# Performance work log

Hardware: AMD Instinct MI355X
Metric: run time of the kernel (lower is better)

## Reference

```python
import jax, jax.numpy as jnp
import numpy as np

B, T, H = 64, 256, 128

def setup_inputs() -> dict:
    key = jax.random.key(0)
    ks = jax.random.split(key, 10)
    s = 1.0 / np.sqrt(H)
    return {
        "x": jax.random.normal(ks[0], (B, T, 2), jnp.float32),
        "enc_output": jax.random.normal(ks[1], (B, T, H), jnp.float32),
        "h0": jax.random.normal(ks[2], (B, H), jnp.float32) * s,
        "c0": jax.random.normal(ks[3], (B, H), jnp.float32) * s,
        "W1": jax.random.normal(ks[4], (H, H), jnp.float32) * s,
        "W2": jax.random.normal(ks[5], (H, H), jnp.float32) * s,
        "V": jax.random.normal(ks[6], (H,), jnp.float32) * s,
        "Wk": jax.random.normal(ks[7], (2, 4 * H), jnp.float32) * (1.0 / np.sqrt(2.0)),
        "Wr": jax.random.normal(ks[8], (H, 4 * H), jnp.float32) * s,
        "b": jnp.zeros((4 * H,), jnp.float32),
    }


def reference(x, enc_output, h0, c0, W1, W2, V, Wk, Wr, b):
    Bb, Tt, _ = x.shape
    # Precompute W1 @ enc_output once (original recomputes it T times inside K.rnn)
    enc_proj = jnp.einsum('bth,hk->btk', enc_output, W1)  # [B,T,H]

    def lstm_cell(inp, h, c):
        # Keras LSTMCell, gate order i,f,c,o; sigmoid recurrent activation, tanh activation
        z = inp @ Wk + h @ Wr + b  # [B,4H]
        zi, zf, zg, zo = jnp.split(z, 4, axis=-1)
        i = jax.nn.sigmoid(zi)
        f = jax.nn.sigmoid(zf)
        g = jnp.tanh(zg)
        o = jax.nn.sigmoid(zo)
        c_new = f * c + i * g
        h_new = o * jnp.tanh(c_new)
        return h_new, c_new

    def step(carry, _):
        h, c, ptr = carry
        h, c = lstm_cell(ptr, h, c)
        # additive attention over all encoder steps, batched (replaces inner K.rnn)
        scores = jnp.einsum('btk,k->bt', jnp.tanh(enc_proj + (h @ W2)[:, None, :]), V)
        probs = jax.nn.softmax(scores, axis=1)  # [B,T]
        # get_pointer with rank=0: top-1 of descending argsort == argmax
        idx = jnp.argmax(probs, axis=1)  # [B]
        ptr = jnp.take_along_axis(x, idx[:, None, None], axis=1)[:, 0, :]  # [B,2]
        return (h, c, ptr), probs

    ptr0 = jnp.ones((Bb, 2), x.dtype)
    _, probs_seq = jax.lax.scan(step, (h0, c0, ptr0), None, length=Tt)  # [T,B,T]
    return jnp.transpose(probs_seq, (1, 0, 2))  # [B,T,T]
```

## Files before the change

### kernel.cpp

```cpp
#include <hip/hip_runtime.h>
#include <cstddef>

#define TT 256
#define HH 128
#define EST 132
#define SCPS 260

__device__ __forceinline__ float rdlane(float v, int l) {
  return __int_as_float(__builtin_amdgcn_readlane(__float_as_int(v), l));
}
__device__ __forceinline__ float fast_sigmoid(float x) {
  const float L2E = 1.4426950408889634f;
  float y = __builtin_amdgcn_exp2f(-x * L2E);
  return __builtin_amdgcn_rcpf(1.0f + y);
}
__device__ __forceinline__ float fast_tanh(float x) {
  const float C2 = 2.8853900817779268f;
  float y = __builtin_amdgcn_exp2f(x * C2);
  return 1.0f - 2.0f * __builtin_amdgcn_rcpf(1.0f + y);
}

__global__ __attribute__((amdgpu_flat_work_group_size(512, 512),
                          amdgpu_waves_per_eu(2, 2)))
void decoder_kernel(const float* __restrict__ x,
                    const float* __restrict__ enc_output,
                    const float* __restrict__ h0,
                    const float* __restrict__ c0,
                    const float* __restrict__ W1,
                    const float* __restrict__ W2,
                    const float* __restrict__ V,
                    const float* __restrict__ Wk,
                    const float* __restrict__ Wr,
                    const float* __restrict__ bias,
                    float* __restrict__ out)
{
  __shared__ float E[TT * EST];
  __shared__ float zpart[4 * 512];
  __shared__ float scp[8 * SCPS];
  __shared__ float hbuf[HH];

  const int u    = threadIdx.x;
  const int b    = blockIdx.x;
  const int lane = u & 63;
  const int w    = u >> 6;
  const float C2  = 2.8853900817779268f;
  const float L2E = 1.4426950408889634f;

  {
    const float* encb = enc_output + (size_t)b * TT * HH;
    const int tsub = u >> 4;
    const int ks   = (u & 15) * 8;
    for (int p = 0; p < 8; ++p) {
      const int tt = p * 32 + tsub;
      float4 a0 = {0.f, 0.f, 0.f, 0.f};
      float4 a1 = {0.f, 0.f, 0.f, 0.f};
      const float4* er4 = (const float4*)(encb + tt * HH);
      for (int j4 = 0; j4 < 32; ++j4) {
        const float4 ev = er4[j4];
        const float* w1p = W1 + (j4 * 4) * HH + ks;
        float4 wa, wb;
        wa = *(const float4*)(w1p + 0 * HH); wb = *(const float4*)(w1p + 0 * HH + 4);
        a0.x += ev.x * wa.x; a0.y += ev.x * wa.y; a0.z += ev.x * wa.z; a0.w += ev.x * wa.w;
        a1.x += ev.x * wb.x; a1.y += ev.x * wb.y; a1.z += ev.x * wb.z; a1.w += ev.x * wb.w;
        wa = *(const float4*)(w1p + 1 * HH); wb = *(const float4*)(w1p + 1 * HH + 4);
        a0.x += ev.y * wa.x; a0.y += ev.y * wa.y; a0.z += ev.y * wa.z; a0.w += ev.y * wa.w;
        a1.x += ev.y * wb.x; a1.y += ev.y * wb.y; a1.z += ev.y * wb.z; a1.w += ev.y * wb.w;
        wa = *(const float4*)(w1p + 2 * HH); wb = *(const float4*)(w1p + 2 * HH + 4);
        a0.x += ev.z * wa.x; a0.y += ev.z * wa.y; a0.z += ev.z * wa.z; a0.w += ev.z * wa.w;
        a1.x += ev.z * wb.x; a1.y += ev.z * wb.y; a1.z += ev.z * wb.z; a1.w += ev.z * wb.w;
        wa = *(const float4*)(w1p + 3 * HH); wb = *(const float4*)(w1p + 3 * HH + 4);
        a0.x += ev.w * wa.x; a0.y += ev.w * wa.y; a0.z += ev.w * wa.z; a0.w += ev.w * wa.w;
        a1.x += ev.w * wb.x; a1.y += ev.w * wb.y; a1.z += ev.w * wb.z; a1.w += ev.w * wb.w;
      }
      *(float4*)(&E[tt * EST + ks])     = a0;
      *(float4*)(&E[tt * EST + ks + 4]) = a1;
    }
  }

  const int kq = u >> 7;
  const int cs = u & 127;
  float4 wr4[32];
  #pragma unroll
  for (int i = 0; i < 32; ++i)
    wr4[i] = *(const float4*)(Wr + (32 * kq + i) * 512 + 4 * cs);
  const int m = 32 * (w & 3) + (lane & 31);
  float wkA[4], wkB[4], bbg[4];
  #pragma unroll
  for (int gg = 0; gg < 4; ++gg) {
    wkA[gg] = Wk[gg * HH + m];
    wkB[gg] = Wk[512 + gg * HH + m];
    bbg[gg] = bias[gg * HH + m];
  }
  float c = c0[b * HH + m];
  float2 xr0 = *(const float2*)(x + b * (TT * 2) + 2 * (0 * 64 + lane));
  float2 xr1 = *(const float2*)(x + b * (TT * 2) + 2 * (1 * 64 + lane));
  float2 xr2 = *(const float2*)(x + b * (TT * 2) + 2 * (2 * 64 + lane));
  float2 xr3 = *(const float2*)(x + b * (TT * 2) + 2 * (3 * 64 + lane));
  const int kk = lane & 15;
  const int jq = lane >> 4;
  float w2local[32];
  #pragma unroll
  for (int i = 0; i < 32; ++i)
    w2local[i] = W2[(32 * jq + i) * HH + 16 * w + kk];
  const float v2r = -2.0f * V[16 * w + kk];
  float vL[16];
  #pragma unroll
  for (int i = 0; i < 16; ++i) vL[i] = rdlane(v2r, i);
  float ptr0 = 1.0f, ptr1 = 1.0f;
  float svr;
  {
    float v = V[lane] + V[64 + lane];
    #pragma unroll
    for (int o = 1; o < 64; o <<= 1) v += __shfl_xor(v, o, 64);
    svr = v;
  }

  __syncthreads();

  {
    float* Er = &E[(u >> 1) * EST + 64 * (u & 1)];
    #pragma unroll
    for (int i = 0; i < 16; ++i) {
      float4 ev = *(const float4*)(Er + 4 * i);
      ev.x = __builtin_amdgcn_exp2f(ev.x * C2);
      ev.y = __builtin_amdgcn_exp2f(ev.y * C2);
      ev.z = __builtin_amdgcn_exp2f(ev.z * C2);
      ev.w = __builtin_amdgcn_exp2f(ev.w * C2);
      *(float4*)(Er + 4 * i) = ev;
    }
  }
  {
    float hA0 = h0[(size_t)b * HH + 32 * kq + (lane & 31)];
    float4 zac = {0.f, 0.f, 0.f, 0.f};
    #pragma unroll
    for (int i = 0; i < 32; ++i) {
      float hi = rdlane(hA0, i);
      zac.x += hi * wr4[i].x;
      zac.y += hi * wr4[i].y;
      zac.z += hi * wr4[i].z;
      zac.w += hi * wr4[i].w;
    }
    *(float4*)(&zpart[kq * 512 + 4 * cs]) = zac;
  }
  __syncthreads();

  float* outb = out + (size_t)b * TT * TT;

  #pragma unroll 1
  for (int step = 0; step < TT; ++step) {
    if (step > 0) {
      float4 sc = {0.f, 0.f, 0.f, 0.f};
      #pragma unroll
      for (int q = 0; q < 8; ++q) {
        float4 v = *(const float4*)(&scp[q * SCPS + 4 * lane]);
        sc.x += v.x; sc.y += v.y; sc.z += v.z; sc.w += v.w;
      }
      if (w < 4) {
        float m4 = fmaxf(fmaxf(sc.x, sc.y), fmaxf(sc.z, sc.w));
        int ttl = (sc.x == m4) ? 0 : (sc.y == m4) ? 1 : (sc.z == m4) ? 2 : 3;
        float mx = m4;
        #pragma unroll
        for (int o = 1; o < 64; o <<= 1) mx = fmaxf(mx, __shfl_xor(mx, o));
        unsigned long long bal = __ballot(m4 == mx);
        int ls  = __ffsll(bal) - 1;
        int tc  = 4 * lane + ttl;
        int tts = __builtin_amdgcn_readlane(tc, ls);
        int j   = tts >> 6;
        int ll  = tts & 63;
        float2 cand = (j == 0) ? xr0 : (j == 1) ? xr1 : (j == 2) ? xr2 : xr3;
        ptr0 = rdlane(cand.x, ll);
        ptr1 = rdlane(cand.y, ll);
      } else {
        sc.x += svr; sc.y += svr; sc.z += svr; sc.w += svr;
        float p0 = __builtin_amdgcn_exp2f((sc.x - 12.0f) * L2E);
        float p1 = __builtin_amdgcn_exp2f((sc.y - 12.0f) * L2E);
        float p2 = __builtin_amdgcn_exp2f((sc.z - 12.0f) * L2E);
        float p3 = __builtin_amdgcn_exp2f((sc.w - 12.0f) * L2E);
        float ws4 = (p0 + p1) + (p2 + p3);
        #pragma unroll
        for (int o = 1; o < 64; o <<= 1) ws4 += __shfl_xor(ws4, o);
        if ((lane >> 4) == (w - 4)) {
          float rs = __builtin_amdgcn_rcpf(ws4);
          float4 po = {p0 * rs, p1 * rs, p2 * rs, p3 * rs};
          *(float4*)(&outb[(size_t)(step - 1) * TT + 4 * lane]) = po;
        }
      }
    }
    if ((lane & 32) == 0 && w < 4) {
      float z0 = bbg[0] + ptr0 * wkA[0] + ptr1 * wkB[0];
      float z1 = bbg[1] + ptr0 * wkA[1] + ptr1 * wkB[1];
      float z2 = bbg[2] + ptr0 * wkA[2] + ptr1 * wkB[2];
      float z3 = bbg[3] + ptr0 * wkA[3] + ptr1 * wkB[3];
      #pragma unroll
      for (int q = 0; q < 4; ++q) {
        z0 += zpart[q * 512 + 0 * HH + m];
        z1 += zpart[q * 512 + 1 * HH + m];
        z2 += zpart[q * 512 + 2 * HH + m];
        z3 += zpart[q * 512 + 3 * HH + m];
      }
      float ig = fast_sigmoid(z0);
      float fg = fast_sigmoid(z1);
      float gg = fast_tanh(z2);
      float og = fast_sigmoid(z3);
      c = fg * c + ig * gg;
      hbuf[m] = og * fast_tanh(c);
    }
    __syncthreads();

    float Uk;
    {
      float cp0 = 0.0f, cp1 = 0.0f;
      const float4* h4 = (const float4*)(hbuf + 32 * jq);
      #pragma unroll
      for (int i4 = 0; i4 < 8; ++i4) {
        float4 hv = h4[i4];
        cp0 += hv.x * w2local[4 * i4 + 0];
        cp1 += hv.y * w2local[4 * i4 + 1];
        cp0 += hv.z * w2local[4 * i4 + 2];
        cp1 += hv.w * w2local[4 * i4 + 3];
      }
      float csum = cp0 + cp1;
      csum += __shfl_xor(csum, 16);
      csum += __shfl_xor(csum, 32);
      Uk = __builtin_amdgcn_exp2f(csum * C2);
    }
    {
      float uL[16];
      #pragma unroll
      for (int i = 0; i < 16; ++i) uL[i] = rdlane(Uk, i);
      #pragma unroll
      for (int tt = 0; tt < 4; ++tt) {
        const float* Er = &E[(64 * tt + lane) * EST + 16 * w];
        float4 e0 = *(const float4*)(Er + 0);
        float4 e1 = *(const float4*)(Er + 4);
        float4 e2 = *(const float4*)(Er + 8);
        float4 e3 = *(const float4*)(Er + 12);
        float a0 = 0.0f, a1 = 0.0f;
        float t0, t1, n;
        t0 = fmaf(e0.x, uL[ 0], 1.0f); t1 = fmaf(e0.y, uL[ 1], 1.0f);
        n  = fmaf(vL[ 1], t0, vL[ 0] * t1);
        a0 = fmaf(n, __builtin_amdgcn_rcpf(t0 * t1), a0);
        t0 = fmaf(e0.z, uL[ 2], 1.0f); t1 = fmaf(e0.w, uL[ 3], 1.0f);
        n  = fmaf(vL[ 3], t0, vL[ 2] * t1);
        a1 = fmaf(n, __builtin_amdgcn_rcpf(t0 * t1), a1);
        t0 = fmaf(e1.x, uL[ 4], 1.0f); t1 = fmaf(e1.y, uL[ 5], 1.0f);
        n  = fmaf(vL[ 5], t0, vL[ 4] * t1);
        a0 = fmaf(n, __builtin_amdgcn_rcpf(t0 * t1), a0);
        t0 = fmaf(e1.z, uL[ 6], 1.0f); t1 = fmaf(e1.w, uL[ 7], 1.0f);
        n  = fmaf(vL[ 7], t0, vL[ 6] * t1);
        a1 = fmaf(n, __builtin_amdgcn_rcpf(t0 * t1), a1);
        t0 = fmaf(e2.x, uL[ 8], 1.0f); t1 = fmaf(e2.y, uL[ 9], 1.0f);
        n  = fmaf(vL[ 9], t0, vL[ 8] * t1);
        a0 = fmaf(n, __builtin_amdgcn_rcpf(t0 * t1), a0);
        t0 = fmaf(e2.z, uL[10], 1.0f); t1 = fmaf(e2.w, uL[11], 1.0f);
        n  = fmaf(vL[11], t0, vL[10] * t1);
        a1 = fmaf(n, __builtin_amdgcn_rcpf(t0 * t1), a1);
        t0 = fmaf(e3.x, uL[12], 1.0f); t1 = fmaf(e3.y, uL[13], 1.0f);
        n  = fmaf(vL[13], t0, vL[12] * t1);
        a0 = fmaf(n, __builtin_amdgcn_rcpf(t0 * t1), a0);
        t0 = fmaf(e3.z, uL[14], 1.0f); t1 = fmaf(e3.w, uL[15], 1.0f);
        n  = fmaf(vL[15], t0, vL[14] * t1);
        a1 = fmaf(n, __builtin_amdgcn_rcpf(t0 * t1), a1);
        scp[w * SCPS + 64 * tt + lane] = a0 + a1;
      }
    }
    {
      const float4* h4 = (const float4*)(hbuf + 32 * kq);
      float4 zac = {0.f, 0.f, 0.f, 0.f};
      #pragma unroll
      for (int i4 = 0; i4 < 8; ++i4) {
        float4 hv = h4[i4];
        zac.x += hv.x * wr4[4 * i4 + 0].x;
        zac.y += hv.x * wr4[4 * i4 + 0].y;
        zac.z += hv.x * wr4[4 * i4 + 0].z;
        zac.w += hv.x * wr4[4 * i4 + 0].w;
        zac.x += hv.y * wr4[4 * i4 + 1].x;
        zac.y += hv.y * wr4[4 * i4 + 1].y;
        zac.z += hv.y * wr4[4 * i4 + 1].z;
        zac.w += hv.y * wr4[4 * i4 + 1].w;
        zac.x += hv.z * wr4[4 * i4 + 2].x;
        zac.y += hv.z * wr4[4 * i4 + 2].y;
        zac.z += hv.z * wr4[4 * i4 + 2].z;
        zac.w += hv.z * wr4[4 * i4 + 2].w;
        zac.x += hv.w * wr4[4 * i4 + 3].x;
        zac.y += hv.w * wr4[4 * i4 + 3].y;
        zac.z += hv.w * wr4[4 * i4 + 3].z;
        zac.w += hv.w * wr4[4 * i4 + 3].w;
      }
      *(float4*)(&zpart[kq * 512 + 4 * cs]) = zac;
    }
    __syncthreads();
  }

  if (w >= 4) {
    float4 sc = {0.f, 0.f, 0.f, 0.f};
    #pragma unroll
    for (int q = 0; q < 8; ++q) {
      float4 v = *(const float4*)(&scp[q * SCPS + 4 * lane]);
      sc.x += v.x; sc.y += v.y; sc.z += v.z; sc.w += v.w;
    }
    sc.x += svr; sc.y += svr; sc.z += svr; sc.w += svr;
    float p0 = __builtin_amdgcn_exp2f((sc.x - 12.0f) * L2E);
    float p1 = __builtin_amdgcn_exp2f((sc.y - 12.0f) * L2E);
    float p2 = __builtin_amdgcn_exp2f((sc.z - 12.0f) * L2E);
    float p3 = __builtin_amdgcn_exp2f((sc.w - 12.0f) * L2E);
    float ws4 = (p0 + p1) + (p2 + p3);
    #pragma unroll
    for (int o = 1; o < 64; o <<= 1) ws4 += __shfl_xor(ws4, o);
    if ((lane >> 4) == (w - 4)) {
      float rs = __builtin_amdgcn_rcpf(ws4);
      float4 po = {p0 * rs, p1 * rs, p2 * rs, p3 * rs};
      *(float4*)(&outb[(size_t)255 * TT + 4 * lane]) = po;
    }
  }
}

extern "C" void kernel_launch(void* const* d_in, const int* in_sizes, int n_in,
                              void* d_out, int out_size, void* d_ws, size_t ws_size,
                              hipStream_t stream) {
  (void)in_sizes; (void)n_in; (void)d_ws; (void)ws_size; (void)out_size;
  const float* x    = (const float*)d_in[0];
  const float* enc  = (const float*)d_in[1];
  const float* h0   = (const float*)d_in[2];
  const float* c0   = (const float*)d_in[3];
  const float* W1   = (const float*)d_in[4];
  const float* W2   = (const float*)d_in[5];
  const float* V    = (const float*)d_in[6];
  const float* Wk   = (const float*)d_in[7];
  const float* Wr   = (const float*)d_in[8];
  const float* bias = (const float*)d_in[9];
  float* out = (float*)d_out;

  decoder_kernel<<<64, 512, 0, stream>>>(x, enc, h0, c0, W1, W2, V, Wk, Wr, bias, out);
}
```

Baseline: 807.7 us.

## Double workgroup to 1024 threads and halve per-thread recurrent and attention work

Launches 1024 threads per batch block instead of 512. Each thread now handles 2 LSTM gate columns instead of 4 and 8 attention hidden units instead of 16, and the partial score buffer grows to 16 slices. The pointer lookup now reads x from shared memory instead of four register-held readlane candidates. The aim is to shorten the serial per-step critical path. The cost is more block-wide barrier participants, more partial sums to reduce each step, and tighter register limits at 4 waves per EU.

```diff
diff --git a/kernel.cpp b/kernel.cpp
--- a/kernel.cpp
+++ b/kernel.cpp
@@ -20,8 +20,8 @@
   return 1.0f - 2.0f * __builtin_amdgcn_rcpf(1.0f + y);
 }
 
-__global__ __attribute__((amdgpu_flat_work_group_size(512, 512),
-                          amdgpu_waves_per_eu(2, 2)))
+__global__ __attribute__((amdgpu_flat_work_group_size(1024, 1024),
+                          amdgpu_waves_per_eu(4, 4)))
 void decoder_kernel(const float* __restrict__ x,
                     const float* __restrict__ enc_output,
                     const float* __restrict__ h0,
@@ -36,8 +36,9 @@
 {
   __shared__ float E[TT * EST];
   __shared__ float zpart[4 * 512];
-  __shared__ float scp[8 * SCPS];
+  __shared__ float scp[16 * SCPS];
   __shared__ float hbuf[HH];
+  __shared__ float xlds[2 * TT];
 
   const int u    = threadIdx.x;
   const int b    = blockIdx.x;
@@ -50,8 +51,8 @@
     const float* encb = enc_output + (size_t)b * TT * HH;
     const int tsub = u >> 4;
     const int ks   = (u & 15) * 8;
-    for (int p = 0; p < 8; ++p) {
-      const int tt = p * 32 + tsub;
+    for (int p = 0; p < 4; ++p) {
+      const int tt = p * 64 + tsub;
       float4 a0 = {0.f, 0.f, 0.f, 0.f};
       float4 a1 = {0.f, 0.f, 0.f, 0.f};
       const float4* er4 = (const float4*)(encb + tt * HH);
@@ -75,14 +76,15 @@
       *(float4*)(&E[tt * EST + ks])     = a0;
       *(float4*)(&E[tt * EST + ks + 4]) = a1;
     }
-  }
-
-  const int kq = u >> 7;
-  const int cs = u & 127;
-  float4 wr4[32];
+    if (u < 2 * TT) xlds[u] = x[b * (TT * 2) + u];
+  }
+
+  const int kq  = u >> 8;
+  const int cs2 = u & 255;
+  float2 wr2[32];
   #pragma unroll
   for (int i = 0; i < 32; ++i)
-    wr4[i] = *(const float4*)(Wr + (32 * kq + i) * 512 + 4 * cs);
+    wr2[i] = *(const float2*)(Wr + (size_t)(32 * kq + i) * 512 + 2 * cs2);
   const int m = 32 * (w & 3) + (lane & 31);
   float wkA[4], wkB[4], bbg[4];
   #pragma unroll
@@ -92,20 +94,16 @@
     bbg[gg] = bias[gg * HH + m];
   }
   float c = c0[b * HH + m];
-  float2 xr0 = *(const float2*)(x + b * (TT * 2) + 2 * (0 * 64 + lane));
-  float2 xr1 = *(const float2*)(x + b * (TT * 2) + 2 * (1 * 64 + lane));
-  float2 xr2 = *(const float2*)(x + b * (TT * 2) + 2 * (2 * 64 + lane));
-  float2 xr3 = *(const float2*)(x + b * (TT * 2) + 2 * (3 * 64 + lane));
-  const int kk = lane & 15;
-  const int jq = lane >> 4;
-  float w2local[32];
+  const int kk8 = lane & 7;
+  const int jq8 = lane >> 3;
+  float w2loc[16];
   #pragma unroll
-  for (int i = 0; i < 32; ++i)
-    w2local[i] = W2[(32 * jq + i) * HH + 16 * w + kk];
-  const float v2r = -2.0f * V[16 * w + kk];
-  float vL[16];
+  for (int i = 0; i < 16; ++i)
+    w2loc[i] = W2[(16 * jq8 + i) * HH + 8 * w + kk8];
+  const float v2r = -2.0f * V[8 * w + kk8];
+  float vL[8];
   #pragma unroll
-  for (int i = 0; i < 16; ++i) vL[i] = rdlane(v2r, i);
+  for (int i = 0; i < 8; ++i) vL[i] = rdlane(v2r, i);
   float ptr0 = 1.0f, ptr1 = 1.0f;
   float svr;
   {
@@ -118,9 +116,9 @@
   __syncthreads();
 
   {
-    float* Er = &E[(u >> 1) * EST + 64 * (u & 1)];
-    #pragma unroll
-    for (int i = 0; i < 16; ++i) {
+    float* Er = &E[(u >> 2) * EST + 32 * (u & 3)];
+    #pragma unroll
+    for (int i = 0; i < 8; ++i) {
       float4 ev = *(const float4*)(Er + 4 * i);
       ev.x = __builtin_amdgcn_exp2f(ev.x * C2);
       ev.y = __builtin_amdgcn_exp2f(ev.y * C2);
@@ -131,16 +129,14 @@
   }
   {
     float hA0 = h0[(size_t)b * HH + 32 * kq + (lane & 31)];
-    float4 zac = {0.f, 0.f, 0.f, 0.f};
+    float2 zac = {0.f, 0.f};
     #pragma unroll
     for (int i = 0; i < 32; ++i) {
       float hi = rdlane(hA0, i);
-      zac.x += hi * wr4[i].x;
-      zac.y += hi * wr4[i].y;
-      zac.z += hi * wr4[i].z;
-      zac.w += hi * wr4[i].w;
-    }
-    *(float4*)(&zpart[kq * 512 + 4 * cs]) = zac;
+      zac.x += hi * wr2[i].x;
+      zac.y += hi * wr2[i].y;
+    }
+    *(float2*)(&zpart[kq * 512 + 2 * cs2]) = zac;
   }
   __syncthreads();
 
@@ -149,13 +145,13 @@
   #pragma unroll 1
   for (int step = 0; step < TT; ++step) {
     if (step > 0) {
-      float4 sc = {0.f, 0.f, 0.f, 0.f};
-      #pragma unroll
-      for (int q = 0; q < 8; ++q) {
-        float4 v = *(const float4*)(&scp[q * SCPS + 4 * lane]);
-        sc.x += v.x; sc.y += v.y; sc.z += v.z; sc.w += v.w;
-      }
       if (w < 4) {
+        float4 sc = {0.f, 0.f, 0.f, 0.f};
+        #pragma unroll
+        for (int q = 0; q < 16; ++q) {
+          const float4 v = *(const float4*)(&scp[q * SCPS + 4 * lane]);
+          sc.x += v.x; sc.y += v.y; sc.z += v.z; sc.w += v.w;
+        }
         float m4 = fmaxf(fmaxf(sc.x, sc.y), fmaxf(sc.z, sc.w));
         int ttl = (sc.x == m4) ? 0 : (sc.y == m4) ? 1 : (sc.z == m4) ? 2 : 3;
         float mx = m4;
@@ -165,12 +161,16 @@
         int ls  = __ffsll(bal) - 1;
         int tc  = 4 * lane + ttl;
         int tts = __builtin_amdgcn_readlane(tc, ls);
-        int j   = tts >> 6;
-        int ll  = tts & 63;
-        float2 cand = (j == 0) ? xr0 : (j == 1) ? xr1 : (j == 2) ? xr2 : xr3;
-        ptr0 = rdlane(cand.x, ll);
-        ptr1 = rdlane(cand.y, ll);
-      } else {
+        const float2 pp = *(const float2*)(&xlds[2 * tts]);
+        ptr0 = pp.x;
+        ptr1 = pp.y;
+      } else if (w < 8) {
+        float4 sc = {0.f, 0.f, 0.f, 0.f};
+        #pragma unroll
+        for (int q = 0; q < 16; ++q) {
+          const float4 v = *(const float4*)(&scp[q * SCPS + 4 * lane]);
+          sc.x += v.x; sc.y += v.y; sc.z += v.z; sc.w += v.w;
+        }
         sc.x += svr; sc.y += svr; sc.z += svr; sc.w += svr;
         float p0 = __builtin_amdgcn_exp2f((sc.x - 12.0f) * L2E);
         float p1 = __builtin_amdgcn_exp2f((sc.y - 12.0f) * L2E);
@@ -210,93 +210,68 @@
     float Uk;
     {
       float cp0 = 0.0f, cp1 = 0.0f;
-      const float4* h4 = (const float4*)(hbuf + 32 * jq);
-      #pragma unroll
-      for (int i4 = 0; i4 < 8; ++i4) {
+      const float4* h4 = (const float4*)(hbuf + 16 * jq8);
+      #pragma unroll
+      for (int i4 = 0; i4 < 4; ++i4) {
         float4 hv = h4[i4];
-        cp0 += hv.x * w2local[4 * i4 + 0];
-        cp1 += hv.y * w2local[4 * i4 + 1];
-        cp0 += hv.z * w2local[4 * i4 + 2];
-        cp1 += hv.w * w2local[4 * i4 + 3];
+        cp0 += hv.x * w2loc[4 * i4 + 0];
+        cp1 += hv.y * w2loc[4 * i4 + 1];
+        cp0 += hv.z * w2loc[4 * i4 + 2];
+        cp1 += hv.w * w2loc[4 * i4 + 3];
       }
       float csum = cp0 + cp1;
+      csum += __shfl_xor(csum, 8);
       csum += __shfl_xor(csum, 16);
       csum += __shfl_xor(csum, 32);
       Uk = __builtin_amdgcn_exp2f(csum * C2);
     }
     {
-      float uL[16];
-      #pragma unroll
-      for (int i = 0; i < 16; ++i) uL[i] = rdlane(Uk, i);
+      float uL[8];
+      #pragma unroll
+      for (int i = 0; i < 8; ++i) uL[i] = rdlane(Uk, i);
       #pragma unroll
       for (int tt = 0; tt < 4; ++tt) {
-        const float* Er = &E[(64 * tt + lane) * EST + 16 * w];
+        const float* Er = &E[(64 * tt + lane) * EST + 8 * w];
         float4 e0 = *(const float4*)(Er + 0);
         float4 e1 = *(const float4*)(Er + 4);
-        float4 e2 = *(const float4*)(Er + 8);
-        float4 e3 = *(const float4*)(Er + 12);
         float a0 = 0.0f, a1 = 0.0f;
         float t0, t1, n;
-        t0 = fmaf(e0.x, uL[ 0], 1.0f); t1 = fmaf(e0.y, uL[ 1], 1.0f);
-        n  = fmaf(vL[ 1], t0, vL[ 0] * t1);
+        t0 = fmaf(e0.x, uL[0], 1.0f); t1 = fmaf(e0.y, uL[1], 1.0f);
+        n  = fmaf(vL[1], t0, vL[0] * t1);
         a0 = fmaf(n, __builtin_amdgcn_rcpf(t0 * t1), a0);
-        t0 = fmaf(e0.z, uL[ 2], 1.0f); t1 = fmaf(e0.w, uL[ 3], 1.0f);
-        n  = fmaf(vL[ 3], t0, vL[ 2] * t1);
+        t0 = fmaf(e0.z, uL[2], 1.0f); t1 = fmaf(e0.w, uL[3], 1.0f);
+        n  = fmaf(vL[3], t0, vL[2] * t1);
         a1 = fmaf(n, __builtin_amdgcn_rcpf(t0 * t1), a1);
-        t0 = fmaf(e1.x, uL[ 4], 1.0f); t1 = fmaf(e1.y, uL[ 5], 1.0f);
-        n  = fmaf(vL[ 5], t0, vL[ 4] * t1);
+        t0 = fmaf(e1.x, uL[4], 1.0f); t1 = fmaf(e1.y, uL[5], 1.0f);
+        n  = fmaf(vL[5], t0, vL[4] * t1);
         a0 = fmaf(n, __builtin_amdgcn_rcpf(t0 * t1), a0);
-        t0 = fmaf(e1.z, uL[ 6], 1.0f); t1 = fmaf(e1.w, uL[ 7], 1.0f);
-        n  = fmaf(vL[ 7], t0, vL[ 6] * t1);
-        a1 = fmaf(n, __builtin_amdgcn_rcpf(t0 * t1), a1);
-        t0 = fmaf(e2.x, uL[ 8], 1.0f); t1 = fmaf(e2.y, uL[ 9], 1.0f);
-        n  = fmaf(vL[ 9], t0, vL[ 8] * t1);
-        a0 = fmaf(n, __builtin_amdgcn_rcpf(t0 * t1), a0);
-        t0 = fmaf(e2.z, uL[10], 1.0f); t1 = fmaf(e2.w, uL[11], 1.0f);
-        n  = fmaf(vL[11], t0, vL[10] * t1);
-        a1 = fmaf(n, __builtin_amdgcn_rcpf(t0 * t1), a1);
-        t0 = fmaf(e3.x, uL[12], 1.0f); t1 = fmaf(e3.y, uL[13], 1.0f);
-        n  = fmaf(vL[13], t0, vL[12] * t1);
-        a0 = fmaf(n, __builtin_amdgcn_rcpf(t0 * t1), a0);
-        t0 = fmaf(e3.z, uL[14], 1.0f); t1 = fmaf(e3.w, uL[15], 1.0f);
-        n  = fmaf(vL[15], t0, vL[14] * t1);
+        t0 = fmaf(e1.z, uL[6], 1.0f); t1 = fmaf(e1.w, uL[7], 1.0f);
+        n  = fmaf(vL[7], t0, vL[6] * t1);
         a1 = fmaf(n, __builtin_amdgcn_rcpf(t0 * t1), a1);
         scp[w * SCPS + 64 * tt + lane] = a0 + a1;
       }
     }
     {
       const float4* h4 = (const float4*)(hbuf + 32 * kq);
-      float4 zac = {0.f, 0.f, 0.f, 0.f};
+      float2 zac = {0.f, 0.f};
       #pragma unroll
       for (int i4 = 0; i4 < 8; ++i4) {
         float4 hv = h4[i4];
-        zac.x += hv.x * wr4[4 * i4 + 0].x;
-        zac.y += hv.x * wr4[4 * i4 + 0].y;
-        zac.z += hv.x * wr4[4 * i4 + 0].z;
-        zac.w += hv.x * wr4[4 * i4 + 0].w;
-        zac.x += hv.y * wr4[4 * i4 + 1].x;
-        zac.y += hv.y * wr4[4 * i4 + 1].y;
-        zac.z += hv.y * wr4[4 * i4 + 1].z;
-        zac.w += hv.y * wr4[4 * i4 + 1].w;
-        zac.x += hv.z * wr4[4 * i4 + 2].x;
-        zac.y += hv.z * wr4[4 * i4 + 2].y;
-        zac.z += hv.z * wr4[4 * i4 + 2].z;
-        zac.w += hv.z * wr4[4 * i4 + 2].w;
-        zac.x += hv.w * wr4[4 * i4 + 3].x;
-        zac.y += hv.w * wr4[4 * i4 + 3].y;
-        zac.z += hv.w * wr4[4 * i4 + 3].z;
-        zac.w += hv.w * wr4[4 * i4 + 3].w;
-      }
-      *(float4*)(&zpart[kq * 512 + 4 * cs]) = zac;
+        zac.x += hv.x * wr2[4 * i4 + 0].x; zac.y += hv.x * wr2[4 * i4 + 0].y;
+        zac.x += hv.y * wr2[4 * i4 + 1].x; zac.y += hv.y * wr2[4 * i4 + 1].y;
+        zac.x += hv.z * wr2[4 * i4 + 2].x; zac.y += hv.z * wr2[4 * i4 + 2].y;
+        zac.x += hv.w * wr2[4 * i4 + 3].x; zac.y += hv.w * wr2[4 * i4 + 3].y;
+      }
+      *(float2*)(&zpart[kq * 512 + 2 * cs2]) = zac;
     }
     __syncthreads();
   }
 
-  if (w >= 4) {
+  if (w >= 4 && w < 8) {
     float4 sc = {0.f, 0.f, 0.f, 0.f};
     #pragma unroll
-    for (int q = 0; q < 8; ++q) {
-      float4 v = *(const float4*)(&scp[q * SCPS + 4 * lane]);
+    for (int q = 0; q < 16; ++q) {
+      const float4 v = *(const float4*)(&scp[q * SCPS + 4 * lane]);
       sc.x += v.x; sc.y += v.y; sc.z += v.z; sc.w += v.w;
     }
     sc.x += svr; sc.y += svr; sc.z += svr; sc.w += svr;
@@ -331,5 +306,5 @@
   const float* bias = (const float*)d_in[9];
   float* out = (float*)d_out;
 
-  decoder_kernel<<<64, 512, 0, stream>>>(x, enc, h0, c0, W1, W2, V, Wk, Wr, bias, out);
-}
+  decoder_kernel<<<64, 1024, 0, stream>>>(x, enc, h0, c0, W1, W2, V, Wk, Wr, bias, out);
+}
```

After: 891.3 us. +10.3%, slower.

## Defer softmax to epilogue, move recurrent matvec earlier, read pointer from LDS

Applied to the files above, without the earlier changes.

The per-step softmax (exp, cross-lane sum reduction, normalize) is replaced inside the serial loop by writing raw score sums to the output. A post-loop pass re-reads each row from global memory and applies a max-stabilized softmax. The Wr recurrent matvec moves ahead of the attention-score block within the step, and the argmax pointer lookup reads x from LDS instead of readlane selects. The goal is to shorten the serial critical path per step, at the cost of an extra global read and write of the output plus a new LDS buffer.

```diff
diff --git a/kernel.cpp b/kernel.cpp
--- a/kernel.cpp
+++ b/kernel.cpp
@@ -38,6 +38,7 @@
   __shared__ float zpart[4 * 512];
   __shared__ float scp[8 * SCPS];
   __shared__ float hbuf[HH];
+  __shared__ float xlds[2 * TT];
 
   const int u    = threadIdx.x;
   const int b    = blockIdx.x;
@@ -75,6 +76,7 @@
       *(float4*)(&E[tt * EST + ks])     = a0;
       *(float4*)(&E[tt * EST + ks + 4]) = a1;
     }
+    xlds[u] = x[b * (TT * 2) + u];
   }
 
   const int kq = u >> 7;
@@ -92,10 +94,6 @@
     bbg[gg] = bias[gg * HH + m];
   }
   float c = c0[b * HH + m];
-  float2 xr0 = *(const float2*)(x + b * (TT * 2) + 2 * (0 * 64 + lane));
-  float2 xr1 = *(const float2*)(x + b * (TT * 2) + 2 * (1 * 64 + lane));
-  float2 xr2 = *(const float2*)(x + b * (TT * 2) + 2 * (2 * 64 + lane));
-  float2 xr3 = *(const float2*)(x + b * (TT * 2) + 2 * (3 * 64 + lane));
   const int kk = lane & 15;
   const int jq = lane >> 4;
   float w2local[32];
@@ -107,13 +105,6 @@
   #pragma unroll
   for (int i = 0; i < 16; ++i) vL[i] = rdlane(v2r, i);
   float ptr0 = 1.0f, ptr1 = 1.0f;
-  float svr;
-  {
-    float v = V[lane] + V[64 + lane];
-    #pragma unroll
-    for (int o = 1; o < 64; o <<= 1) v += __shfl_xor(v, o, 64);
-    svr = v;
-  }
 
   __syncthreads();
 
@@ -149,13 +140,13 @@
   #pragma unroll 1
   for (int step = 0; step < TT; ++step) {
     if (step > 0) {
-      float4 sc = {0.f, 0.f, 0.f, 0.f};
-      #pragma unroll
-      for (int q = 0; q < 8; ++q) {
-        float4 v = *(const float4*)(&scp[q * SCPS + 4 * lane]);
-        sc.x += v.x; sc.y += v.y; sc.z += v.z; sc.w += v.w;
-      }
       if (w < 4) {
+        float4 sc = {0.f, 0.f, 0.f, 0.f};
+        #pragma unroll
+        for (int q = 0; q < 8; ++q) {
+          float4 v = *(const float4*)(&scp[q * SCPS + 4 * lane]);
+          sc.x += v.x; sc.y += v.y; sc.z += v.z; sc.w += v.w;
+        }
         float m4 = fmaxf(fmaxf(sc.x, sc.y), fmaxf(sc.z, sc.w));
         int ttl = (sc.x == m4) ? 0 : (sc.y == m4) ? 1 : (sc.z == m4) ? 2 : 3;
         float mx = m4;
@@ -165,25 +156,15 @@
         int ls  = __ffsll(bal) - 1;
         int tc  = 4 * lane + ttl;
         int tts = __builtin_amdgcn_readlane(tc, ls);
-        int j   = tts >> 6;
-        int ll  = tts & 63;
-        float2 cand = (j == 0) ? xr0 : (j == 1) ? xr1 : (j == 2) ? xr2 : xr3;
-        ptr0 = rdlane(cand.x, ll);
-        ptr1 = rdlane(cand.y, ll);
+        const float2 pp = *(const float2*)(&xlds[2 * tts]);
+        ptr0 = pp.x;
+        ptr1 = pp.y;
       } else {
-        sc.x += svr; sc.y += svr; sc.z += svr; sc.w += svr;
-        float p0 = __builtin_amdgcn_exp2f((sc.x - 12.0f) * L2E);
-        float p1 = __builtin_amdgcn_exp2f((sc.y - 12.0f) * L2E);
-        float p2 = __builtin_amdgcn_exp2f((sc.z - 12.0f) * L2E);
-        float p3 = __builtin_amdgcn_exp2f((sc.w - 12.0f) * L2E);
-        float ws4 = (p0 + p1) + (p2 + p3);
+        const int t = 64 * (w - 4) + lane;
+        float s = scp[0 * SCPS + t];
         #pragma unroll
-        for (int o = 1; o < 64; o <<= 1) ws4 += __shfl_xor(ws4, o);
-        if ((lane >> 4) == (w - 4)) {
-          float rs = __builtin_amdgcn_rcpf(ws4);
-          float4 po = {p0 * rs, p1 * rs, p2 * rs, p3 * rs};
-          *(float4*)(&outb[(size_t)(step - 1) * TT + 4 * lane]) = po;
-        }
+        for (int q = 1; q < 8; ++q) s += scp[q * SCPS + t];
+        outb[(size_t)(step - 1) * TT + t] = s;
       }
     }
     if ((lane & 32) == 0 && w < 4) {
@@ -223,6 +204,31 @@
       csum += __shfl_xor(csum, 16);
       csum += __shfl_xor(csum, 32);
       Uk = __builtin_amdgcn_exp2f(csum * C2);
+    }
+    {
+      const float4* h4 = (const float4*)(hbuf + 32 * kq);
+      float4 zac = {0.f, 0.f, 0.f, 0.f};
+      #pragma unroll
+      for (int i4 = 0; i4 < 8; ++i4) {
+        float4 hv = h4[i4];
+        zac.x += hv.x * wr4[4 * i4 + 0].x;
+        zac.y += hv.x * wr4[4 * i4 + 0].y;
+        zac.z += hv.x * wr4[4 * i4 + 0].z;
+        zac.w += hv.x * wr4[4 * i4 + 0].w;
+        zac.x += hv.y * wr4[4 * i4 + 1].x;
+        zac.y += hv.y * wr4[4 * i4 + 1].y;
+        zac.z += hv.y * wr4[4 * i4 + 1].z;
+        zac.w += hv.y * wr4[4 * i4 + 1].w;
+        zac.x += hv.z * wr4[4 * i4 + 2].x;
+        zac.y += hv.z * wr4[4 * i4 + 2].y;
+        zac.z += hv.z * wr4[4 * i4 + 2].z;
+        zac.w += hv.z * wr4[4 * i4 + 2].w;
+        zac.x += hv.w * wr4[4 * i4 + 3].x;
+        zac.y += hv.w * wr4[4 * i4 + 3].y;
+        zac.z += hv.w * wr4[4 * i4 + 3].z;
+        zac.w += hv.w * wr4[4 * i4 + 3].w;
+      }
+      *(float4*)(&zpart[kq * 512 + 4 * cs]) = zac;
     }
     {
       float uL[16];
@@ -264,53 +270,36 @@
         scp[w * SCPS + 64 * tt + lane] = a0 + a1;
       }
     }
-    {
-      const float4* h4 = (const float4*)(hbuf + 32 * kq);
-      float4 zac = {0.f, 0.f, 0.f, 0.f};
-      #pragma unroll
-      for (int i4 = 0; i4 < 8; ++i4) {
-        float4 hv = h4[i4];
-        zac.x += hv.x * wr4[4 * i4 + 0].x;
-        zac.y += hv.x * wr4[4 * i4 + 0].y;
-        zac.z += hv.x * wr4[4 * i4 + 0].z;
-        zac.w += hv.x * wr4[4 * i4 + 0].w;
-        zac.x += hv.y * wr4[4 * i4 + 1].x;
-        zac.y += hv.y * wr4[4 * i4 + 1].y;
-        zac.z += hv.y * wr4[4 * i4 + 1].z;
-        zac.w += hv.y * wr4[4 * i4 + 1].w;
-        zac.x += hv.z * wr4[4 * i4 + 2].x;
-        zac.y += hv.z * wr4[4 * i4 + 2].y;
-        zac.z += hv.z * wr4[4 * i4 + 2].z;
-        zac.w += hv.z * wr4[4 * i4 + 2].w;
-        zac.x += hv.w * wr4[4 * i4 + 3].x;
-        zac.y += hv.w * wr4[4 * i4 + 3].y;
-        zac.z += hv.w * wr4[4 * i4 + 3].z;
-        zac.w += hv.w * wr4[4 * i4 + 3].w;
-      }
-      *(float4*)(&zpart[kq * 512 + 4 * cs]) = zac;
-    }
     __syncthreads();
   }
 
   if (w >= 4) {
-    float4 sc = {0.f, 0.f, 0.f, 0.f};
+    const int t = 64 * (w - 4) + lane;
+    float s = scp[0 * SCPS + t];
     #pragma unroll
-    for (int q = 0; q < 8; ++q) {
-      float4 v = *(const float4*)(&scp[q * SCPS + 4 * lane]);
-      sc.x += v.x; sc.y += v.y; sc.z += v.z; sc.w += v.w;
-    }
-    sc.x += svr; sc.y += svr; sc.z += svr; sc.w += svr;
-    float p0 = __builtin_amdgcn_exp2f((sc.x - 12.0f) * L2E);
-    float p1 = __builtin_amdgcn_exp2f((sc.y - 12.0f) * L2E);
-    float p2 = __builtin_amdgcn_exp2f((sc.z - 12.0f) * L2E);
-    float p3 = __builtin_amdgcn_exp2f((sc.w - 12.0f) * L2E);
-    float ws4 = (p0 + p1) + (p2 + p3);
-    #pragma unroll
-    for (int o = 1; o < 64; o <<= 1) ws4 += __shfl_xor(ws4, o);
-    if ((lane >> 4) == (w - 4)) {
-      float rs = __builtin_amdgcn_rcpf(ws4);
+    for (int q = 1; q < 8; ++q) s += scp[q * SCPS + t];
+    outb[(size_t)255 * TT + t] = s;
+  }
+  __syncthreads();
+
+  {
+    #pragma unroll 2
+    for (int i = 0; i < 32; ++i) {
+      float* rp = outb + (size_t)(32 * w + i) * TT;
+      float4 v = *(const float4*)(rp + 4 * lane);
+      float mx = fmaxf(fmaxf(v.x, v.y), fmaxf(v.z, v.w));
+      #pragma unroll
+      for (int o = 1; o < 64; o <<= 1) mx = fmaxf(mx, __shfl_xor(mx, o));
+      float p0 = __builtin_amdgcn_exp2f((v.x - mx) * L2E);
+      float p1 = __builtin_amdgcn_exp2f((v.y - mx) * L2E);
+      float p2 = __builtin_amdgcn_exp2f((v.z - mx) * L2E);
+      float p3 = __builtin_amdgcn_exp2f((v.w - mx) * L2E);
+      float ws = (p0 + p1) + (p2 + p3);
+      #pragma unroll
+      for (int o = 1; o < 64; o <<= 1) ws += __shfl_xor(ws, o);
+      float rs = __builtin_amdgcn_rcpf(ws);
       float4 po = {p0 * rs, p1 * rs, p2 * rs, p3 * rs};
-      *(float4*)(&outb[(size_t)255 * TT + 4 * lane]) = po;
+      *(float4*)(rp + 4 * lane) = po;
     }
   }
 }
```

New measurement: 851.0 us. 1.05x slower.

## Use packed FP32 FMAs, LDS pointer lookup, and readlane-based recurrent matvec

Applied to the files above, without the earlier changes.

Rewrites the enc projection, W2 projection, Wr recurrent matvec and attention t-terms to use two-wide packed FMA (v_pk_fma_f32). The pointer gather now reads x from LDS instead of selecting among four registers with readlanes. The recurrent matvec now broadcasts h via readlane from a per-lane float2 and runs before the attention loop. The scp reduction is split per branch. These changes aim to halve VALU issue count in the hot step loop and cut register use. The cost is extra LDS and packing moves.

```diff
diff --git a/kernel.cpp b/kernel.cpp
--- a/kernel.cpp
+++ b/kernel.cpp
@@ -5,6 +5,11 @@
 #define HH 128
 #define EST 132
 #define SCPS 260
+
+typedef float f2 __attribute__((ext_vector_type(2)));
+
+__device__ __forceinline__ f2 mkf2(float a, float b) { f2 r; r.x = a; r.y = b; return r; }
+__device__ __forceinline__ f2 pkfma(f2 a, f2 b, f2 c) { return __builtin_elementwise_fma(a, b, c); }
 
 __device__ __forceinline__ float rdlane(float v, int l) {
   return __int_as_float(__builtin_amdgcn_readlane(__float_as_int(v), l));
@@ -38,6 +43,7 @@
   __shared__ float zpart[4 * 512];
   __shared__ float scp[8 * SCPS];
   __shared__ float hbuf[HH];
+  __shared__ float xlds[2 * TT];
 
   const int u    = threadIdx.x;
   const int b    = blockIdx.x;
@@ -45,6 +51,7 @@
   const int w    = u >> 6;
   const float C2  = 2.8853900817779268f;
   const float L2E = 1.4426950408889634f;
+  const f2 one2 = {1.0f, 1.0f};
 
   {
     const float* encb = enc_output + (size_t)b * TT * HH;
@@ -52,32 +59,41 @@
     const int ks   = (u & 15) * 8;
     for (int p = 0; p < 8; ++p) {
       const int tt = p * 32 + tsub;
-      float4 a0 = {0.f, 0.f, 0.f, 0.f};
-      float4 a1 = {0.f, 0.f, 0.f, 0.f};
+      f2 a0l = {0.f, 0.f}, a0h = {0.f, 0.f};
+      f2 a1l = {0.f, 0.f}, a1h = {0.f, 0.f};
       const float4* er4 = (const float4*)(encb + tt * HH);
       for (int j4 = 0; j4 < 32; ++j4) {
         const float4 ev = er4[j4];
         const float* w1p = W1 + (j4 * 4) * HH + ks;
         float4 wa, wb;
+        f2 s;
         wa = *(const float4*)(w1p + 0 * HH); wb = *(const float4*)(w1p + 0 * HH + 4);
-        a0.x += ev.x * wa.x; a0.y += ev.x * wa.y; a0.z += ev.x * wa.z; a0.w += ev.x * wa.w;
-        a1.x += ev.x * wb.x; a1.y += ev.x * wb.y; a1.z += ev.x * wb.z; a1.w += ev.x * wb.w;
+        s = mkf2(ev.x, ev.x);
+        a0l = pkfma(s, mkf2(wa.x, wa.y), a0l); a0h = pkfma(s, mkf2(wa.z, wa.w), a0h);
+        a1l = pkfma(s, mkf2(wb.x, wb.y), a1l); a1h = pkfma(s, mkf2(wb.z, wb.w), a1h);
         wa = *(const float4*)(w1p + 1 * HH); wb = *(const float4*)(w1p + 1 * HH + 4);
-        a0.x += ev.y * wa.x; a0.y += ev.y * wa.y; a0.z += ev.y * wa.z; a0.w += ev.y * wa.w;
-        a1.x += ev.y * wb.x; a1.y += ev.y * wb.y; a1.z += ev.y * wb.z; a1.w += ev.y * wb.w;
+        s = mkf2(ev.y, ev.y);
+        a0l = pkfma(s, mkf2(wa.x, wa.y), a0l); a0h = pkfma(s, mkf2(wa.z, wa.w), a0h);
+        a1l = pkfma(s, mkf2(wb.x, wb.y), a1l); a1h = pkfma(s, mkf2(wb.z, wb.w), a1h);
         wa = *(const float4*)(w1p + 2 * HH); wb = *(const float4*)(w1p + 2 * HH + 4);
-        a0.x += ev.z * wa.x; a0.y += ev.z * wa.y; a0.z += ev.z * wa.z; a0.w += ev.z * wa.w;
-        a1.x += ev.z * wb.x; a1.y += ev.z * wb.y; a1.z += ev.z * wb.z; a1.w += ev.z * wb.w;
+        s = mkf2(ev.z, ev.z);
+        a0l = pkfma(s, mkf2(wa.x, wa.y), a0l); a0h = pkfma(s, mkf2(wa.z, wa.w), a0h);
+        a1l = pkfma(s, mkf2(wb.x, wb.y), a1l); a1h = pkfma(s, mkf2(wb.z, wb.w), a1h);
         wa = *(const float4*)(w1p + 3 * HH); wb = *(const float4*)(w1p + 3 * HH + 4);
-        a0.x += ev.w * wa.x; a0.y += ev.w * wa.y; a0.z += ev.w * wa.z; a0.w += ev.w * wa.w;
-        a1.x += ev.w * wb.x; a1.y += ev.w * wb.y; a1.z += ev.w * wb.z; a1.w += ev.w * wb.w;
-      }
-      *(float4*)(&E[tt * EST + ks])     = a0;
-      *(float4*)(&E[tt * EST + ks + 4]) = a1;
-    }
+        s = mkf2(ev.w, ev.w);
+        a0l = pkfma(s, mkf2(wa.x, wa.y), a0l); a0h = pkfma(s, mkf2(wa.z, wa.w), a0h);
+        a1l = pkfma(s, mkf2(wb.x, wb.y), a1l); a1h = pkfma(s, mkf2(wb.z, wb.w), a1h);
+      }
+      float4 o0 = {a0l.x, a0l.y, a0h.x, a0h.y};
+      float4 o1 = {a1l.x, a1l.y, a1h.x, a1h.y};
+      *(float4*)(&E[tt * EST + ks])     = o0;
+      *(float4*)(&E[tt * EST + ks + 4]) = o1;
+    }
+    xlds[u] = x[b * (TT * 2) + u];
   }
 
   const int kq = u >> 7;
+  const int kqs = __builtin_amdgcn_readfirstlane(kq);
   const int cs = u & 127;
   float4 wr4[32];
   #pragma unroll
@@ -92,16 +108,13 @@
     bbg[gg] = bias[gg * HH + m];
   }
   float c = c0[b * HH + m];
-  float2 xr0 = *(const float2*)(x + b * (TT * 2) + 2 * (0 * 64 + lane));
-  float2 xr1 = *(const float2*)(x + b * (TT * 2) + 2 * (1 * 64 + lane));
-  float2 xr2 = *(const float2*)(x + b * (TT * 2) + 2 * (2 * 64 + lane));
-  float2 xr3 = *(const float2*)(x + b * (TT * 2) + 2 * (3 * 64 + lane));
   const int kk = lane & 15;
   const int jq = lane >> 4;
-  float w2local[32];
+  f2 w2f2[16];
   #pragma unroll
-  for (int i = 0; i < 32; ++i)
-    w2local[i] = W2[(32 * jq + i) * HH + 16 * w + kk];
+  for (int i = 0; i < 16; ++i)
+    w2f2[i] = mkf2(W2[(32 * jq + 2 * i) * HH + 16 * w + kk],
+                   W2[(32 * jq + 2 * i + 1) * HH + 16 * w + kk]);
   const float v2r = -2.0f * V[16 * w + kk];
   float vL[16];
   #pragma unroll
@@ -131,16 +144,16 @@
   }
   {
     float hA0 = h0[(size_t)b * HH + 32 * kq + (lane & 31)];
-    float4 zac = {0.f, 0.f, 0.f, 0.f};
+    f2 zacl = {0.f, 0.f}, zach = {0.f, 0.f};
     #pragma unroll
     for (int i = 0; i < 32; ++i) {
       float hi = rdlane(hA0, i);
-      zac.x += hi * wr4[i].x;
-      zac.y += hi * wr4[i].y;
-      zac.z += hi * wr4[i].z;
-      zac.w += hi * wr4[i].w;
-    }
-    *(float4*)(&zpart[kq * 512 + 4 * cs]) = zac;
+      f2 h2 = mkf2(hi, hi);
+      zacl = pkfma(h2, mkf2(wr4[i].x, wr4[i].y), zacl);
+      zach = pkfma(h2, mkf2(wr4[i].z, wr4[i].w), zach);
+    }
+    float4 zo = {zacl.x, zacl.y, zach.x, zach.y};
+    *(float4*)(&zpart[kq * 512 + 4 * cs]) = zo;
   }
   __syncthreads();
 
@@ -149,13 +162,13 @@
   #pragma unroll 1
   for (int step = 0; step < TT; ++step) {
     if (step > 0) {
-      float4 sc = {0.f, 0.f, 0.f, 0.f};
-      #pragma unroll
-      for (int q = 0; q < 8; ++q) {
-        float4 v = *(const float4*)(&scp[q * SCPS + 4 * lane]);
-        sc.x += v.x; sc.y += v.y; sc.z += v.z; sc.w += v.w;
-      }
       if (w < 4) {
+        float4 sc = {0.f, 0.f, 0.f, 0.f};
+        #pragma unroll
+        for (int q = 0; q < 8; ++q) {
+          float4 v = *(const float4*)(&scp[q * SCPS + 4 * lane]);
+          sc.x += v.x; sc.y += v.y; sc.z += v.z; sc.w += v.w;
+        }
         float m4 = fmaxf(fmaxf(sc.x, sc.y), fmaxf(sc.z, sc.w));
         int ttl = (sc.x == m4) ? 0 : (sc.y == m4) ? 1 : (sc.z == m4) ? 2 : 3;
         float mx = m4;
@@ -165,12 +178,16 @@
         int ls  = __ffsll(bal) - 1;
         int tc  = 4 * lane + ttl;
         int tts = __builtin_amdgcn_readlane(tc, ls);
-        int j   = tts >> 6;
-        int ll  = tts & 63;
-        float2 cand = (j == 0) ? xr0 : (j == 1) ? xr1 : (j == 2) ? xr2 : xr3;
-        ptr0 = rdlane(cand.x, ll);
-        ptr1 = rdlane(cand.y, ll);
+        const float2 pp = *(const float2*)(&xlds[2 * tts]);
+        ptr0 = pp.x;
+        ptr1 = pp.y;
       } else {
+        float4 sc = {0.f, 0.f, 0.f, 0.f};
+        #pragma unroll
+        for (int q = 0; q < 8; ++q) {
+          float4 v = *(const float4*)(&scp[q * SCPS + 4 * lane]);
+          sc.x += v.x; sc.y += v.y; sc.z += v.z; sc.w += v.w;
+        }
         sc.x += svr; sc.y += svr; sc.z += svr; sc.w += svr;
         float p0 = __builtin_amdgcn_exp2f((sc.x - 12.0f) * L2E);
         float p1 = __builtin_amdgcn_exp2f((sc.y - 12.0f) * L2E);
@@ -208,26 +225,44 @@
     __syncthreads();
 
     float Uk;
+    f2 h2own;
     {
-      float cp0 = 0.0f, cp1 = 0.0f;
+      h2own = *(const f2*)(hbuf + 2 * lane);
+      f2 cpv = {0.f, 0.f};
       const float4* h4 = (const float4*)(hbuf + 32 * jq);
       #pragma unroll
       for (int i4 = 0; i4 < 8; ++i4) {
         float4 hv = h4[i4];
-        cp0 += hv.x * w2local[4 * i4 + 0];
-        cp1 += hv.y * w2local[4 * i4 + 1];
-        cp0 += hv.z * w2local[4 * i4 + 2];
-        cp1 += hv.w * w2local[4 * i4 + 3];
-      }
-      float csum = cp0 + cp1;
+        cpv = pkfma(mkf2(hv.x, hv.y), w2f2[2 * i4],     cpv);
+        cpv = pkfma(mkf2(hv.z, hv.w), w2f2[2 * i4 + 1], cpv);
+      }
+      float csum = cpv.x + cpv.y;
       csum += __shfl_xor(csum, 16);
       csum += __shfl_xor(csum, 32);
       Uk = __builtin_amdgcn_exp2f(csum * C2);
     }
     {
+      f2 zacl = {0.f, 0.f}, zach = {0.f, 0.f};
+      #pragma unroll
+      for (int i2 = 0; i2 < 16; ++i2) {
+        float hx = rdlane(h2own.x, kqs * 16 + i2);
+        float hy = rdlane(h2own.y, kqs * 16 + i2);
+        f2 hx2 = mkf2(hx, hx), hy2 = mkf2(hy, hy);
+        zacl = pkfma(hx2, mkf2(wr4[2 * i2].x,     wr4[2 * i2].y),     zacl);
+        zach = pkfma(hx2, mkf2(wr4[2 * i2].z,     wr4[2 * i2].w),     zach);
+        zacl = pkfma(hy2, mkf2(wr4[2 * i2 + 1].x, wr4[2 * i2 + 1].y), zacl);
+        zach = pkfma(hy2, mkf2(wr4[2 * i2 + 1].z, wr4[2 * i2 + 1].w), zach);
+      }
+      float4 zo = {zacl.x, zacl.y, zach.x, zach.y};
+      *(float4*)(&zpart[kq * 512 + 4 * cs]) = zo;
+    }
+    {
       float uL[16];
       #pragma unroll
       for (int i = 0; i < 16; ++i) uL[i] = rdlane(Uk, i);
+      f2 uf2[8];
+      #pragma unroll
+      for (int j = 0; j < 8; ++j) uf2[j] = mkf2(uL[2 * j], uL[2 * j + 1]);
       #pragma unroll
       for (int tt = 0; tt < 4; ++tt) {
         const float* Er = &E[(64 * tt + lane) * EST + 16 * w];
@@ -236,58 +271,34 @@
         float4 e2 = *(const float4*)(Er + 8);
         float4 e3 = *(const float4*)(Er + 12);
         float a0 = 0.0f, a1 = 0.0f;
-        float t0, t1, n;
-        t0 = fmaf(e0.x, uL[ 0], 1.0f); t1 = fmaf(e0.y, uL[ 1], 1.0f);
-        n  = fmaf(vL[ 1], t0, vL[ 0] * t1);
-        a0 = fmaf(n, __builtin_amdgcn_rcpf(t0 * t1), a0);
-        t0 = fmaf(e0.z, uL[ 2], 1.0f); t1 = fmaf(e0.w, uL[ 3], 1.0f);
-        n  = fmaf(vL[ 3], t0, vL[ 2] * t1);
-        a1 = fmaf(n, __builtin_amdgcn_rcpf(t0 * t1), a1);
-        t0 = fmaf(e1.x, uL[ 4], 1.0f); t1 = fmaf(e1.y, uL[ 5], 1.0f);
-        n  = fmaf(vL[ 5], t0, vL[ 4] * t1);
-        a0 = fmaf(n, __builtin_amdgcn_rcpf(t0 * t1), a0);
-        t0 = fmaf(e1.z, uL[ 6], 1.0f); t1 = fmaf(e1.w, uL[ 7], 1.0f);
-        n  = fmaf(vL[ 7], t0, vL[ 6] * t1);
-        a1 = fmaf(n, __builtin_amdgcn_rcpf(t0 * t1), a1);
-        t0 = fmaf(e2.x, uL[ 8], 1.0f); t1 = fmaf(e2.y, uL[ 9], 1.0f);
-        n  = fmaf(vL[ 9], t0, vL[ 8] * t1);
-        a0 = fmaf(n, __builtin_amdgcn_rcpf(t0 * t1), a0);
-        t0 = fmaf(e2.z, uL[10], 1.0f); t1 = fmaf(e2.w, uL[11], 1.0f);
-        n  = fmaf(vL[11], t0, vL[10] * t1);
-        a1 = fmaf(n, __builtin_amdgcn_rcpf(t0 * t1), a1);
-        t0 = fmaf(e3.x, uL[12], 1.0f); t1 = fmaf(e3.y, uL[13], 1.0f);
-        n  = fmaf(vL[13], t0, vL[12] * t1);
-        a0 = fmaf(n, __builtin_amdgcn_rcpf(t0 * t1), a0);
-        t0 = fmaf(e3.z, uL[14], 1.0f); t1 = fmaf(e3.w, uL[15], 1.0f);
-        n  = fmaf(vL[15], t0, vL[14] * t1);
-        a1 = fmaf(n, __builtin_amdgcn_rcpf(t0 * t1), a1);
+        f2 tp;
+        float n;
+        tp = pkfma(mkf2(e0.x, e0.y), uf2[0], one2);
+        n  = fmaf(vL[ 1], tp.x, vL[ 0] * tp.y);
+        a0 = fmaf(n, __builtin_amdgcn_rcpf(tp.x * tp.y), a0);
+        tp = pkfma(mkf2(e0.z, e0.w), uf2[1], one2);
+        n  = fmaf(vL[ 3], tp.x, vL[ 2] * tp.y);
+        a1 = fmaf(n, __builtin_amdgcn_rcpf(tp.x * tp.y), a1);
+        tp = pkfma(mkf2(e1.x, e1.y), uf2[2], one2);
+        n  = fmaf(vL[ 5], tp.x, vL[ 4] * tp.y);
+        a0 = fmaf(n, __builtin_amdgcn_rcpf(tp.x * tp.y), a0);
+        tp = pkfma(mkf2(e1.z, e1.w), uf2[3], one2);
+        n  = fmaf(vL[ 7], tp.x, vL[ 6] * tp.y);
+        a1 = fmaf(n, __builtin_amdgcn_rcpf(tp.x * tp.y), a1);
+        tp = pkfma(mkf2(e2.x, e2.y), uf2[4], one2);
+        n  = fmaf(vL[ 9], tp.x, vL[ 8] * tp.y);
+        a0 = fmaf(n, __builtin_amdgcn_rcpf(tp.x * tp.y), a0);
+        tp = pkfma(mkf2(e2.z, e2.w), uf2[5], one2);
+        n  = fmaf(vL[11], tp.x, vL[10] * tp.y);
+        a1 = fmaf(n, __builtin_amdgcn_rcpf(tp.x * tp.y), a1);
+        tp = pkfma(mkf2(e3.x, e3.y), uf2[6], one2);
+        n  = fmaf(vL[13], tp.x, vL[12] * tp.y);
+        a0 = fmaf(n, __builtin_amdgcn_rcpf(tp.x * tp.y), a0);
+        tp = pkfma(mkf2(e3.z, e3.w), uf2[7], one2);
+        n  = fmaf(vL[15], tp.x, vL[14] * tp.y);
+        a1 = fmaf(n, __builtin_amdgcn_rcpf(tp.x * tp.y), a1);
         scp[w * SCPS + 64 * tt + lane] = a0 + a1;
       }
-    }
-    {
-      const float4* h4 = (const float4*)(hbuf + 32 * kq);
-      float4 zac = {0.f, 0.f, 0.f, 0.f};
-      #pragma unroll
-      for (int i4 = 0; i4 < 8; ++i4) {
-        float4 hv = h4[i4];
-        zac.x += hv.x * wr4[4 * i4 + 0].x;
-        zac.y += hv.x * wr4[4 * i4 + 0].y;
-        zac.z += hv.x * wr4[4 * i4 + 0].z;
-        zac.w += hv.x * wr4[4 * i4 + 0].w;
-        zac.x += hv.y * wr4[4 * i4 + 1].x;
-        zac.y += hv.y * wr4[4 * i4 + 1].y;
-        zac.z += hv.y * wr4[4 * i4 + 1].z;
-        zac.w += hv.y * wr4[4 * i4 + 1].w;
-        zac.x += hv.z * wr4[4 * i4 + 2].x;
-        zac.y += hv.z * wr4[4 * i4 + 2].y;
-        zac.z += hv.z * wr4[4 * i4 + 2].z;
-        zac.w += hv.z * wr4[4 * i4 + 2].w;
-        zac.x += hv.w * wr4[4 * i4 + 3].x;
-        zac.y += hv.w * wr4[4 * i4 + 3].y;
-        zac.z += hv.w * wr4[4 * i4 + 3].z;
-        zac.w += hv.w * wr4[4 * i4 + 3].w;
-      }
-      *(float4*)(&zpart[kq * 512 + 4 * cs]) = zac;
     }
     __syncthreads();
   }
```

Measured after the change: 856.3 us. 6.0% more time.
